# Optimization experiments

Measured on AMD Instinct MI355X. Metric: run time of the kernel, lower is better.

The kernel has to match this reference:

```python
import jax, jax.numpy as jnp
import numpy as np

EMB_DIM = 768
QKV_DIM = 64
NUM_HEAD = 12


def setup_inputs() -> dict:
    key = jax.random.key(0)
    k1, k2, k3 = jax.random.split(key, 3)
    z = jax.random.normal(k1, (16, 1024, EMB_DIM), dtype=jnp.float32)
    U_qkv = jax.random.normal(k2, (NUM_HEAD, 3, EMB_DIM, QKV_DIM), dtype=jnp.float32) * (1.0 / np.sqrt(EMB_DIM))
    U_msa = jax.random.normal(k3, (NUM_HEAD * QKV_DIM, EMB_DIM), dtype=jnp.float32) * (1.0 / np.sqrt(NUM_HEAD * QKV_DIM))
    return {"z": z, "U_qkv": U_qkv, "U_msa": U_msa}


def reference(z, U_qkv, U_msa):
    # z: [b, n, e]; U_qkv: [h, 3, e, d]; U_msa: [h*d, e]
    qkv = jnp.einsum("bne,hked->khbnd", z, U_qkv)  # [3, h, b, n, d]
    q, k, v = qkv[0], qkv[1], qkv[2]               # each [h, b, n, d]
    scale = 1.0 / jnp.sqrt(jnp.asarray(q.shape[-1], dtype=z.dtype))
    logits = jnp.einsum("hbnd,hbmd->hbnm", q, k) * scale  # [h, b, n, n]
    attn = jax.nn.softmax(logits, axis=-1)
    o = jnp.einsum("hbnm,hbmd->bnhd", attn, v)     # [b, n, h, d]
    b, n = o.shape[0], o.shape[1]
    o = o.reshape(b, n, -1)                        # [b, n, h*d]
    return o @ U_msa                               # [b, n, e]
```

## Files before the change

### kernel.cpp

```cpp
#include <hip/hip_runtime.h>
#include <hip/hip_bf16.h>

typedef _Float16 f16x8 __attribute__((ext_vector_type(8)));
typedef _Float16 f16x4 __attribute__((ext_vector_type(4)));
typedef float f32x4 __attribute__((ext_vector_type(4)));

#define MFMA32(a, b, c) __builtin_amdgcn_mfma_f32_16x16x32_f16(a, b, c, 0, 0, 0)
#define MFMA16(a, b, c) __builtin_amdgcn_mfma_f32_16x16x16f16(a, b, c, 0, 0, 0)

#define GLOAD_LDS16(g, l)                                         \
  __builtin_amdgcn_global_load_lds(                               \
      (const __attribute__((address_space(1))) void*)(g),         \
      (__attribute__((address_space(3))) void*)(l), 16, 0, 0)

__global__ __launch_bounds__(256) void tconv_kernel(
    const float* __restrict__ in, _Float16* __restrict__ out, int R, int C) {
  size_t bat = (size_t)blockIdx.y * R * C;
  int o = blockIdx.x * 256 + threadIdx.x;
  if (o < R * C) {
    int c = o / R, r = o - c * R;
    out[bat + o] = (_Float16)in[bat + (size_t)r * C + c];
  }
}

__global__ __launch_bounds__(256) void cvt16_kernel(
    const float* __restrict__ in, _Float16* __restrict__ out, int n) {
  int i = (blockIdx.x * 256 + threadIdx.x) * 8;
  if (i < n) {
    float4 a = *(const float4*)(in + i);
    float4 b = *(const float4*)(in + i + 4);
    f16x8 cv;
    cv[0] = (_Float16)a.x; cv[1] = (_Float16)a.y;
    cv[2] = (_Float16)a.z; cv[3] = (_Float16)a.w;
    cv[4] = (_Float16)b.x; cv[5] = (_Float16)b.y;
    cv[6] = (_Float16)b.z; cv[7] = (_Float16)b.w;
    *(f16x8*)(out + i) = cv;
  }
}

__global__ __launch_bounds__(256) void qkv_gemm_kernel(
    const _Float16* __restrict__ zh, const _Float16* __restrict__ Ut,
    _Float16* __restrict__ Qf, _Float16* __restrict__ Kf,
    _Float16* __restrict__ Vt) {
  __shared__ _Float16 As[128 * 64];
  __shared__ _Float16 Bs[128 * 64];

  const int tid = threadIdx.x;
  const int wv = tid >> 6, lane = tid & 63, quad = lane >> 4, l16 = lane & 15;

  const int m0 = blockIdx.x * 128;
  const int by = blockIdx.y;
  const int n0 = by * 128;

  const int srow = lane >> 3;
  const int scol = ((lane & 7) ^ srow) << 3;
  const _Float16* Ag = zh + (size_t)(m0 + srow) * 768 + scol;
  const _Float16* Bg = Ut + (size_t)(n0 + srow) * 768 + scol;

  const int cbq = quad * 16;

  f32x4 acc[2][8] = {};

  for (int k0 = 0; k0 < 768; k0 += 64) {
    __syncthreads();
#pragma unroll
    for (int i = 0; i < 4; ++i) {
      const int rb = (i * 4 + wv) * 8;
      GLOAD_LDS16(Ag + (size_t)rb * 768 + k0, (char*)As + rb * 128);
      GLOAD_LDS16(Bg + (size_t)rb * 768 + k0, (char*)Bs + rb * 128);
    }
    __syncthreads();
#pragma unroll
    for (int ks = 0; ks < 2; ++ks) {
      f16x8 af[2], bfr[8];
#pragma unroll
      for (int rt = 0; rt < 2; ++rt) {
        const int r = wv * 32 + rt * 16 + l16;
        af[rt] = *(const f16x8*)((const char*)As + r * 128 +
                                 ((ks * 64 + cbq) ^ ((r & 7) << 4)));
      }
#pragma unroll
      for (int ct = 0; ct < 8; ++ct) {
        const int r = ct * 16 + l16;
        bfr[ct] = *(const f16x8*)((const char*)Bs + r * 128 +
                                  ((ks * 64 + cbq) ^ ((r & 7) << 4)));
      }
#pragma unroll
      for (int rt = 0; rt < 2; ++rt)
#pragma unroll
        for (int ct = 0; ct < 8; ++ct)
          acc[rt][ct] = MFMA32(af[rt], bfr[ct], acc[rt][ct]);
    }
  }

#pragma unroll
  for (int ct = 0; ct < 8; ++ct) {
    const int g = by * 2 + (ct >> 2);
    const int h = g / 3, kk = g - h * 3;
    const int dd = (ct & 3) * 16 + l16;
#pragma unroll
    for (int rt = 0; rt < 2; ++rt) {
#pragma unroll
      for (int r = 0; r < 4; ++r) {
        int m = m0 + wv * 32 + rt * 16 + quad * 4 + r;
        int b = m >> 10, n = m & 1023;
        _Float16 val = (_Float16)acc[rt][ct][r];
        if (kk == 0)
          Qf[(((size_t)h * 16 + b) * 1024 + n) * 64 + dd] = val;
        else if (kk == 1)
          Kf[(((size_t)h * 16 + b) * 1024 + n) * 64 + dd] = val;
        else
          Vt[(((size_t)h * 16 + b) * 64 + dd) * 1024 + n] = val;
      }
    }
  }
}

__global__ __launch_bounds__(256) void attn_kernel(
    const _Float16* __restrict__ Qf, const _Float16* __restrict__ Kf,
    const _Float16* __restrict__ Vt, _Float16* __restrict__ Of) {
  __shared__ _Float16 Ks[2][64][72];
  __shared__ _Float16 Vs[2][64][72];

  const int tid = threadIdx.x;
  const int wv = tid >> 6, lane = tid & 63, quad = lane >> 4, l16 = lane & 15;

  const int flat = blockIdx.x;
  const int swz = (flat & 7) * 192 + (flat >> 3);
  const int hb = swz >> 3;
  const int h = hb >> 4, b = hb & 15;
  const _Float16* Q = Qf + (size_t)hb * 65536;
  const _Float16* K = Kf + (size_t)hb * 65536;
  const _Float16* V = Vt + (size_t)hb * 65536;
  const int q0 = (swz & 7) * 128 + wv * 32;

  const _Float16 cs = (_Float16)0.18033688011112042f;
  f16x8 qfr[2][2];
#pragma unroll
  for (int mi = 0; mi < 2; ++mi) {
    const _Float16* qp = Q + (size_t)(q0 + mi * 16 + l16) * 64 + quad * 8;
    qfr[mi][0] = *(const f16x8*)qp * cs;
    qfr[mi][1] = *(const f16x8*)(qp + 32) * cs;
  }

  const int r0 = tid >> 3, c0 = (tid & 7) << 3;
  const _Float16* Kst = K + (size_t)r0 * 64 + c0;
  const _Float16* Vst = V + (size_t)r0 * 1024 + c0;

  uint4 kreg[2], vreg[2];
#pragma unroll
  for (int i = 0; i < 2; ++i) {
    kreg[i] = *(const uint4*)(Kst + i * 2048);
    vreg[i] = *(const uint4*)(Vst + i * 32768);
  }
#pragma unroll
  for (int i = 0; i < 2; ++i) {
    *(uint4*)&Ks[0][r0 + i * 32][c0] = kreg[i];
    *(uint4*)&Vs[0][r0 + i * 32][c0] = vreg[i];
  }
  __syncthreads();

  f32x4 o[2][4] = {};
  float lsum[2] = {};

  for (int t = 0; t < 16; ++t) {
    const int cur = t & 1;
    if (t < 15) {
      int n1 = (t + 1) * 64;
#pragma unroll
      for (int i = 0; i < 2; ++i) {
        kreg[i] = *(const uint4*)(Kst + (size_t)n1 * 64 + i * 2048);
        vreg[i] = *(const uint4*)(Vst + n1 + i * 32768);
      }
    }

    f32x4 st[2][4] = {};
    __builtin_amdgcn_s_setprio(1);
#pragma unroll
    for (int ct = 0; ct < 4; ++ct) {
      f16x8 kf0 = *(const f16x8*)&Ks[cur][ct * 16 + l16][quad * 8];
      f16x8 kf1 = *(const f16x8*)&Ks[cur][ct * 16 + l16][32 + quad * 8];
#pragma unroll
      for (int mi = 0; mi < 2; ++mi) {
        st[mi][ct] = MFMA32(kf0, qfr[mi][0], st[mi][ct]);
        st[mi][ct] = MFMA32(kf1, qfr[mi][1], st[mi][ct]);
      }
    }
    __builtin_amdgcn_s_setprio(0);

    f16x4 pa[2][4];
#pragma unroll
    for (int mi = 0; mi < 2; ++mi)
#pragma unroll
      for (int ct = 0; ct < 4; ++ct)
#pragma unroll
        for (int r = 0; r < 4; ++r) {
          float p = __builtin_amdgcn_exp2f(st[mi][ct][r]);
          lsum[mi] += p;
          pa[mi][ct][r] = (_Float16)p;
        }

    __builtin_amdgcn_s_setprio(1);
#pragma unroll
    for (int dt = 0; dt < 4; ++dt) {
#pragma unroll
      for (int kb = 0; kb < 4; ++kb) {
        f16x4 vf = *(const f16x4*)&Vs[cur][dt * 16 + l16][kb * 16 + quad * 4];
#pragma unroll
        for (int mi = 0; mi < 2; ++mi)
          o[mi][dt] = MFMA16(pa[mi][kb], vf, o[mi][dt]);
      }
    }
    __builtin_amdgcn_s_setprio(0);

    if (t < 15) {
#pragma unroll
      for (int i = 0; i < 2; ++i) {
        *(uint4*)&Ks[cur ^ 1][r0 + i * 32][c0] = kreg[i];
        *(uint4*)&Vs[cur ^ 1][r0 + i * 32][c0] = vreg[i];
      }
      __syncthreads();
    }
  }

#pragma unroll
  for (int mi = 0; mi < 2; ++mi) {
    float s = lsum[mi];
    s += __shfl_xor(s, 16, 64);
    s += __shfl_xor(s, 32, 64);
    lsum[mi] = s;
  }

#pragma unroll
  for (int mi = 0; mi < 2; ++mi) {
#pragma unroll
    for (int r = 0; r < 4; ++r) {
      float inv = 1.f / __shfl(lsum[mi], quad * 4 + r, 64);
      int n = q0 + mi * 16 + quad * 4 + r;
#pragma unroll
      for (int dt = 0; dt < 4; ++dt) {
        int dd = dt * 16 + l16;
        __builtin_nontemporal_store(
            (_Float16)(o[mi][dt][r] * inv),
            &Of[((size_t)b * 1024 + n) * 768 + h * 64 + dd]);
      }
    }
  }
}

__global__ __launch_bounds__(256) void out_gemm_kernel(
    const _Float16* __restrict__ A, const _Float16* __restrict__ Bt,
    float* __restrict__ Cout) {
  __shared__ _Float16 As[128 * 64];
  __shared__ _Float16 Bs[128 * 64];

  const int tid = threadIdx.x;
  const int wv = tid >> 6, lane = tid & 63, quad = lane >> 4, l16 = lane & 15;

  const int m0 = blockIdx.x * 128;
  const int n0 = blockIdx.y * 128;

  const int srow = lane >> 3;
  const int scol = ((lane & 7) ^ srow) << 3;
  const _Float16* Ag = A + (size_t)(m0 + srow) * 768 + scol;
  const _Float16* Bg = Bt + (size_t)(n0 + srow) * 768 + scol;

  const int cbq = quad * 16;

  f32x4 acc[2][8] = {};

  for (int k0 = 0; k0 < 768; k0 += 64) {
    __syncthreads();
#pragma unroll
    for (int i = 0; i < 4; ++i) {
      const int rb = (i * 4 + wv) * 8;
      GLOAD_LDS16(Ag + (size_t)rb * 768 + k0, (char*)As + rb * 128);
      GLOAD_LDS16(Bg + (size_t)rb * 768 + k0, (char*)Bs + rb * 128);
    }
    __syncthreads();
#pragma unroll
    for (int ks = 0; ks < 2; ++ks) {
      f16x8 af[2], bfr[8];
#pragma unroll
      for (int rt = 0; rt < 2; ++rt) {
        const int r = wv * 32 + rt * 16 + l16;
        af[rt] = *(const f16x8*)((const char*)As + r * 128 +
                                 ((ks * 64 + cbq) ^ ((r & 7) << 4)));
      }
#pragma unroll
      for (int ct = 0; ct < 8; ++ct) {
        const int r = ct * 16 + l16;
        bfr[ct] = *(const f16x8*)((const char*)Bs + r * 128 +
                                  ((ks * 64 + cbq) ^ ((r & 7) << 4)));
      }
#pragma unroll
      for (int rt = 0; rt < 2; ++rt)
#pragma unroll
        for (int ct = 0; ct < 8; ++ct)
          acc[rt][ct] = MFMA32(af[rt], bfr[ct], acc[rt][ct]);
    }
  }

#pragma unroll
  for (int rt = 0; rt < 2; ++rt) {
#pragma unroll
    for (int ct = 0; ct < 8; ++ct) {
#pragma unroll
      for (int r = 0; r < 4; ++r) {
        int m = m0 + wv * 32 + rt * 16 + quad * 4 + r;
        int n = n0 + ct * 16 + l16;
        __builtin_nontemporal_store(acc[rt][ct][r],
                                    &Cout[(size_t)m * 768 + n]);
      }
    }
  }
}

extern "C" void kernel_launch(void* const* d_in, const int* in_sizes, int n_in,
                              void* d_out, int out_size, void* d_ws,
                              size_t ws_size, hipStream_t stream) {
  const float* z = (const float*)d_in[0];
  const float* Uqkv = (const float*)d_in[1];
  const float* Umsa = (const float*)d_in[2];

  char* ws = (char*)d_ws;
  _Float16* Ut_qkv = (_Float16*)(ws);
  _Float16* Ut_msa = (_Float16*)(ws + 3538944);
  _Float16* zh = (_Float16*)(ws + 4718592);
  _Float16* Of = zh;
  _Float16* Qf = (_Float16*)(ws + 29884416);
  _Float16* Kf = (_Float16*)(ws + 55050240);
  _Float16* Vt = (_Float16*)(ws + 80216064);

  tconv_kernel<<<dim3(192, 36), 256, 0, stream>>>(Uqkv, Ut_qkv, 768, 64);
  tconv_kernel<<<dim3(2304, 1), 256, 0, stream>>>(Umsa, Ut_msa, 768, 768);
  cvt16_kernel<<<dim3(6144, 1), 256, 0, stream>>>(z, zh, 16384 * 768);

  qkv_gemm_kernel<<<dim3(128, 18), 256, 0, stream>>>(zh, Ut_qkv, Qf, Kf, Vt);
  attn_kernel<<<dim3(1536, 1), 256, 0, stream>>>(Qf, Kf, Vt, Of);
  out_gemm_kernel<<<dim3(128, 6), 256, 0, stream>>>(Of, Ut_msa,
                                                    (float*)d_out);
}
```

Baseline: 358.4 us.

## Double-buffer LDS tiles in QKV and output GEMMs to overlap loads with MFMA

```diff
diff --git a/kernel.cpp b/kernel.cpp
--- a/kernel.cpp
+++ b/kernel.cpp
@@ -42,8 +42,8 @@
     const _Float16* __restrict__ zh, const _Float16* __restrict__ Ut,
     _Float16* __restrict__ Qf, _Float16* __restrict__ Kf,
     _Float16* __restrict__ Vt) {
-  __shared__ _Float16 As[128 * 64];
-  __shared__ _Float16 Bs[128 * 64];
+  __shared__ _Float16 As[2][128 * 64];
+  __shared__ _Float16 Bs[2][128 * 64];
 
   const int tid = threadIdx.x;
   const int wv = tid >> 6, lane = tid & 63, quad = lane >> 4, l16 = lane & 15;
@@ -61,28 +61,41 @@
 
   f32x4 acc[2][8] = {};
 
-  for (int k0 = 0; k0 < 768; k0 += 64) {
-    __syncthreads();
-#pragma unroll
-    for (int i = 0; i < 4; ++i) {
-      const int rb = (i * 4 + wv) * 8;
-      GLOAD_LDS16(Ag + (size_t)rb * 768 + k0, (char*)As + rb * 128);
-      GLOAD_LDS16(Bg + (size_t)rb * 768 + k0, (char*)Bs + rb * 128);
-    }
-    __syncthreads();
+#pragma unroll
+  for (int i = 0; i < 4; ++i) {
+    const int rb = (i * 4 + wv) * 8;
+    GLOAD_LDS16(Ag + (size_t)rb * 768, (char*)As[0] + rb * 128);
+    GLOAD_LDS16(Bg + (size_t)rb * 768, (char*)Bs[0] + rb * 128);
+  }
+  asm volatile("s_waitcnt vmcnt(0)" ::: "memory");
+  __builtin_amdgcn_s_barrier();
+
+  for (int t = 0; t < 12; ++t) {
+    const int cur = t & 1;
+    if (t < 11) {
+      const int k1 = (t + 1) * 64;
+#pragma unroll
+      for (int i = 0; i < 4; ++i) {
+        const int rb = (i * 4 + wv) * 8;
+        GLOAD_LDS16(Ag + (size_t)rb * 768 + k1,
+                    (char*)As[cur ^ 1] + rb * 128);
+        GLOAD_LDS16(Bg + (size_t)rb * 768 + k1,
+                    (char*)Bs[cur ^ 1] + rb * 128);
+      }
+    }
 #pragma unroll
     for (int ks = 0; ks < 2; ++ks) {
       f16x8 af[2], bfr[8];
 #pragma unroll
       for (int rt = 0; rt < 2; ++rt) {
         const int r = wv * 32 + rt * 16 + l16;
-        af[rt] = *(const f16x8*)((const char*)As + r * 128 +
+        af[rt] = *(const f16x8*)((const char*)As[cur] + r * 128 +
                                  ((ks * 64 + cbq) ^ ((r & 7) << 4)));
       }
 #pragma unroll
       for (int ct = 0; ct < 8; ++ct) {
         const int r = ct * 16 + l16;
-        bfr[ct] = *(const f16x8*)((const char*)Bs + r * 128 +
+        bfr[ct] = *(const f16x8*)((const char*)Bs[cur] + r * 128 +
                                   ((ks * 64 + cbq) ^ ((r & 7) << 4)));
       }
 #pragma unroll
@@ -90,6 +103,10 @@
 #pragma unroll
         for (int ct = 0; ct < 8; ++ct)
           acc[rt][ct] = MFMA32(af[rt], bfr[ct], acc[rt][ct]);
+    }
+    if (t < 11) {
+      asm volatile("s_waitcnt vmcnt(0)" ::: "memory");
+      __builtin_amdgcn_s_barrier();
     }
   }
 
@@ -251,8 +268,8 @@
 __global__ __launch_bounds__(256) void out_gemm_kernel(
     const _Float16* __restrict__ A, const _Float16* __restrict__ Bt,
     float* __restrict__ Cout) {
-  __shared__ _Float16 As[128 * 64];
-  __shared__ _Float16 Bs[128 * 64];
+  __shared__ _Float16 As[2][128 * 64];
+  __shared__ _Float16 Bs[2][128 * 64];
 
   const int tid = threadIdx.x;
   const int wv = tid >> 6, lane = tid & 63, quad = lane >> 4, l16 = lane & 15;
@@ -269,28 +286,41 @@
 
   f32x4 acc[2][8] = {};
 
-  for (int k0 = 0; k0 < 768; k0 += 64) {
-    __syncthreads();
-#pragma unroll
-    for (int i = 0; i < 4; ++i) {
-      const int rb = (i * 4 + wv) * 8;
-      GLOAD_LDS16(Ag + (size_t)rb * 768 + k0, (char*)As + rb * 128);
-      GLOAD_LDS16(Bg + (size_t)rb * 768 + k0, (char*)Bs + rb * 128);
-    }
-    __syncthreads();
+#pragma unroll
+  for (int i = 0; i < 4; ++i) {
+    const int rb = (i * 4 + wv) * 8;
+    GLOAD_LDS16(Ag + (size_t)rb * 768, (char*)As[0] + rb * 128);
+    GLOAD_LDS16(Bg + (size_t)rb * 768, (char*)Bs[0] + rb * 128);
+  }
+  asm volatile("s_waitcnt vmcnt(0)" ::: "memory");
+  __builtin_amdgcn_s_barrier();
+
+  for (int t = 0; t < 12; ++t) {
+    const int cur = t & 1;
+    if (t < 11) {
+      const int k1 = (t + 1) * 64;
+#pragma unroll
+      for (int i = 0; i < 4; ++i) {
+        const int rb = (i * 4 + wv) * 8;
+        GLOAD_LDS16(Ag + (size_t)rb * 768 + k1,
+                    (char*)As[cur ^ 1] + rb * 128);
+        GLOAD_LDS16(Bg + (size_t)rb * 768 + k1,
+                    (char*)Bs[cur ^ 1] + rb * 128);
+      }
+    }
 #pragma unroll
     for (int ks = 0; ks < 2; ++ks) {
       f16x8 af[2], bfr[8];
 #pragma unroll
       for (int rt = 0; rt < 2; ++rt) {
         const int r = wv * 32 + rt * 16 + l16;
-        af[rt] = *(const f16x8*)((const char*)As + r * 128 +
+        af[rt] = *(const f16x8*)((const char*)As[cur] + r * 128 +
                                  ((ks * 64 + cbq) ^ ((r & 7) << 4)));
       }
 #pragma unroll
       for (int ct = 0; ct < 8; ++ct) {
         const int r = ct * 16 + l16;
-        bfr[ct] = *(const f16x8*)((const char*)Bs + r * 128 +
+        bfr[ct] = *(const f16x8*)((const char*)Bs[cur] + r * 128 +
                                   ((ks * 64 + cbq) ^ ((r & 7) << 4)));
       }
 #pragma unroll
@@ -298,6 +328,10 @@
 #pragma unroll
         for (int ct = 0; ct < 8; ++ct)
           acc[rt][ct] = MFMA32(af[rt], bfr[ct], acc[rt][ct]);
+    }
+    if (t < 11) {
+      asm volatile("s_waitcnt vmcnt(0)" ::: "memory");
+      __builtin_amdgcn_s_barrier();
     }
   }
 
```

Result: faster. 347.6 us (-3.0%).

## Load attention K/V fragments directly from global; double-buffer output GEMM LDS

Applied to the files above, without the earlier changes.

```diff
diff --git a/kernel.cpp b/kernel.cpp
--- a/kernel.cpp
+++ b/kernel.cpp
@@ -119,9 +119,6 @@
 __global__ __launch_bounds__(256) void attn_kernel(
     const _Float16* __restrict__ Qf, const _Float16* __restrict__ Kf,
     const _Float16* __restrict__ Vt, _Float16* __restrict__ Of) {
-  __shared__ _Float16 Ks[2][64][72];
-  __shared__ _Float16 Vs[2][64][72];
-
   const int tid = threadIdx.x;
   const int wv = tid >> 6, lane = tid & 63, quad = lane >> 4, l16 = lane & 15;
 
@@ -143,50 +140,37 @@
     qfr[mi][1] = *(const f16x8*)(qp + 32) * cs;
   }
 
-  const int r0 = tid >> 3, c0 = (tid & 7) << 3;
-  const _Float16* Kst = K + (size_t)r0 * 64 + c0;
-  const _Float16* Vst = V + (size_t)r0 * 1024 + c0;
-
-  uint4 kreg[2], vreg[2];
-#pragma unroll
-  for (int i = 0; i < 2; ++i) {
-    kreg[i] = *(const uint4*)(Kst + i * 2048);
-    vreg[i] = *(const uint4*)(Vst + i * 32768);
-  }
-#pragma unroll
-  for (int i = 0; i < 2; ++i) {
-    *(uint4*)&Ks[0][r0 + i * 32][c0] = kreg[i];
-    *(uint4*)&Vs[0][r0 + i * 32][c0] = vreg[i];
-  }
-  __syncthreads();
+  const _Float16* Kfr = K + (size_t)l16 * 64 + quad * 8;
+  const _Float16* Vfr = V + (size_t)l16 * 1024 + quad * 4;
 
   f32x4 o[2][4] = {};
   float lsum[2] = {};
 
   for (int t = 0; t < 16; ++t) {
-    const int cur = t & 1;
-    if (t < 15) {
-      int n1 = (t + 1) * 64;
-#pragma unroll
-      for (int i = 0; i < 2; ++i) {
-        kreg[i] = *(const uint4*)(Kst + (size_t)n1 * 64 + i * 2048);
-        vreg[i] = *(const uint4*)(Vst + n1 + i * 32768);
-      }
-    }
+    f16x8 kf[4][2];
+#pragma unroll
+    for (int ct = 0; ct < 4; ++ct)
+#pragma unroll
+      for (int ks = 0; ks < 2; ++ks)
+        kf[ct][ks] =
+            *(const f16x8*)(Kfr + (size_t)(t * 64 + ct * 16) * 64 + ks * 32);
 
     f32x4 st[2][4] = {};
-    __builtin_amdgcn_s_setprio(1);
-#pragma unroll
-    for (int ct = 0; ct < 4; ++ct) {
-      f16x8 kf0 = *(const f16x8*)&Ks[cur][ct * 16 + l16][quad * 8];
-      f16x8 kf1 = *(const f16x8*)&Ks[cur][ct * 16 + l16][32 + quad * 8];
+#pragma unroll
+    for (int ct = 0; ct < 4; ++ct)
 #pragma unroll
       for (int mi = 0; mi < 2; ++mi) {
-        st[mi][ct] = MFMA32(kf0, qfr[mi][0], st[mi][ct]);
-        st[mi][ct] = MFMA32(kf1, qfr[mi][1], st[mi][ct]);
-      }
-    }
-    __builtin_amdgcn_s_setprio(0);
+        st[mi][ct] = MFMA32(kf[ct][0], qfr[mi][0], st[mi][ct]);
+        st[mi][ct] = MFMA32(kf[ct][1], qfr[mi][1], st[mi][ct]);
+      }
+
+    f16x4 vf[4][4];
+#pragma unroll
+    for (int dt = 0; dt < 4; ++dt)
+#pragma unroll
+      for (int kb = 0; kb < 4; ++kb)
+        vf[dt][kb] =
+            *(const f16x4*)(Vfr + (size_t)dt * 16384 + t * 64 + kb * 16);
 
     f16x4 pa[2][4];
 #pragma unroll
@@ -200,27 +184,13 @@
           pa[mi][ct][r] = (_Float16)p;
         }
 
-    __builtin_amdgcn_s_setprio(1);
-#pragma unroll
-    for (int dt = 0; dt < 4; ++dt) {
-#pragma unroll
-      for (int kb = 0; kb < 4; ++kb) {
-        f16x4 vf = *(const f16x4*)&Vs[cur][dt * 16 + l16][kb * 16 + quad * 4];
+#pragma unroll
+    for (int dt = 0; dt < 4; ++dt)
+#pragma unroll
+      for (int kb = 0; kb < 4; ++kb)
 #pragma unroll
         for (int mi = 0; mi < 2; ++mi)
-          o[mi][dt] = MFMA16(pa[mi][kb], vf, o[mi][dt]);
-      }
-    }
-    __builtin_amdgcn_s_setprio(0);
-
-    if (t < 15) {
-#pragma unroll
-      for (int i = 0; i < 2; ++i) {
-        *(uint4*)&Ks[cur ^ 1][r0 + i * 32][c0] = kreg[i];
-        *(uint4*)&Vs[cur ^ 1][r0 + i * 32][c0] = vreg[i];
-      }
-      __syncthreads();
-    }
+          o[mi][dt] = MFMA16(pa[mi][kb], vf[dt][kb], o[mi][dt]);
   }
 
 #pragma unroll
@@ -251,8 +221,8 @@
 __global__ __launch_bounds__(256) void out_gemm_kernel(
     const _Float16* __restrict__ A, const _Float16* __restrict__ Bt,
     float* __restrict__ Cout) {
-  __shared__ _Float16 As[128 * 64];
-  __shared__ _Float16 Bs[128 * 64];
+  __shared__ _Float16 As[2][128 * 64];
+  __shared__ _Float16 Bs[2][128 * 64];
 
   const int tid = threadIdx.x;
   const int wv = tid >> 6, lane = tid & 63, quad = lane >> 4, l16 = lane & 15;
@@ -269,28 +239,41 @@
 
   f32x4 acc[2][8] = {};
 
-  for (int k0 = 0; k0 < 768; k0 += 64) {
-    __syncthreads();
-#pragma unroll
-    for (int i = 0; i < 4; ++i) {
-      const int rb = (i * 4 + wv) * 8;
-      GLOAD_LDS16(Ag + (size_t)rb * 768 + k0, (char*)As + rb * 128);
-      GLOAD_LDS16(Bg + (size_t)rb * 768 + k0, (char*)Bs + rb * 128);
-    }
-    __syncthreads();
+#pragma unroll
+  for (int i = 0; i < 4; ++i) {
+    const int rb = (i * 4 + wv) * 8;
+    GLOAD_LDS16(Ag + (size_t)rb * 768, (char*)As[0] + rb * 128);
+    GLOAD_LDS16(Bg + (size_t)rb * 768, (char*)Bs[0] + rb * 128);
+  }
+  asm volatile("s_waitcnt vmcnt(0)" ::: "memory");
+  __builtin_amdgcn_s_barrier();
+
+  for (int t = 0; t < 12; ++t) {
+    const int cur = t & 1;
+    if (t < 11) {
+      const int k1 = (t + 1) * 64;
+#pragma unroll
+      for (int i = 0; i < 4; ++i) {
+        const int rb = (i * 4 + wv) * 8;
+        GLOAD_LDS16(Ag + (size_t)rb * 768 + k1,
+                    (char*)As[cur ^ 1] + rb * 128);
+        GLOAD_LDS16(Bg + (size_t)rb * 768 + k1,
+                    (char*)Bs[cur ^ 1] + rb * 128);
+      }
+    }
 #pragma unroll
     for (int ks = 0; ks < 2; ++ks) {
       f16x8 af[2], bfr[8];
 #pragma unroll
       for (int rt = 0; rt < 2; ++rt) {
         const int r = wv * 32 + rt * 16 + l16;
-        af[rt] = *(const f16x8*)((const char*)As + r * 128 +
+        af[rt] = *(const f16x8*)((const char*)As[cur] + r * 128 +
                                  ((ks * 64 + cbq) ^ ((r & 7) << 4)));
       }
 #pragma unroll
       for (int ct = 0; ct < 8; ++ct) {
         const int r = ct * 16 + l16;
-        bfr[ct] = *(const f16x8*)((const char*)Bs + r * 128 +
+        bfr[ct] = *(const f16x8*)((const char*)Bs[cur] + r * 128 +
                                   ((ks * 64 + cbq) ^ ((r & 7) << 4)));
       }
 #pragma unroll
@@ -298,6 +281,10 @@
 #pragma unroll
         for (int ct = 0; ct < 8; ++ct)
           acc[rt][ct] = MFMA32(af[rt], bfr[ct], acc[rt][ct]);
+    }
+    if (t < 11) {
+      asm volatile("s_waitcnt vmcnt(0)" ::: "memory");
+      __builtin_amdgcn_s_barrier();
     }
   }
 
```

Result: slower. 518.5 us (+44.7%).
